# Kernel optimization log

Measured on AMD Instinct MI355X. Metric: run time of the kernel, lower is better.

The kernel has to match this reference:

```python
import jax, jax.numpy as jnp
import numpy as np

B, T, IN_CH, OUT_CH = 4, 512, 128, 128
NEG_INF = -1e22  # same large negative as the torch module


def setup_inputs() -> dict:
    key = jax.random.key(0)
    kx, ka, kq, kk, kp = jax.random.split(key, 5)
    x = jax.random.normal(kx, (B, T, IN_CH), dtype=jnp.float32)
    adj = jax.random.normal(ka, (B, T, T), dtype=jnp.float32)  # >0 -> edge
    # xavier-uniform-like scale for Linear weights (stored as (in, out) so y = x @ W)
    s_qk = float(np.sqrt(6.0 / (IN_CH + OUT_CH)))
    WQ = jax.random.uniform(kq, (IN_CH, OUT_CH), jnp.float32, -s_qk, s_qk)
    WK = jax.random.uniform(kk, (IN_CH, OUT_CH), jnp.float32, -s_qk, s_qk)
    s_p = float(np.sqrt(6.0 / (OUT_CH + 1)))
    p = jax.random.uniform(kp, (OUT_CH,), jnp.float32, -s_p, s_p)  # proj_att weight
    return {"x": x, "adj": adj, "WQ": WQ, "WK": WK, "p": p}


def reference(x, adj, WQ, WK, p):
    """Faithful LGCN forward (eval mode: dropout is identity).

    att[b,i,j] = p . relu(q[b,j] + k[b,i])   (note torch indexing:
    feat_q broadcast over dim 1, feat_k broadcast over dim 2)
    out[b,i]  = sum_j softmax_j(att + mask)[b,i,j] * x[b,j]
    """
    mask = jnp.where(adj > 0, jnp.float32(0.0), jnp.float32(NEG_INF))  # (B,T,T)
    q = x @ WQ  # (B,T,O)
    k = x @ WK  # (B,T,O)
    # (B, T_i, T_j, O): q indexed by j, k indexed by i
    h = jax.nn.relu(q[:, None, :, :] + k[:, :, None, :])
    score = jnp.einsum("bijd,d->bij", h, p)  # (B,T,T)
    att = jax.nn.softmax(score + mask, axis=-1)
    return jnp.matmul(att, x)  # (B,T,IN_CH)
```

## Files before the change

kernel.cpp:

```cpp
#include <hip/hip_runtime.h>

#define B_ 4
#define T_ 512
#define C_ 128
#define NEG_INF_ (-1e22f)
#define QSTRIDE 20

__global__ __launch_bounds__(256) void qk_gemm(const float* __restrict__ x,
                                               const float* __restrict__ WQ,
                                               const float* __restrict__ WK,
                                               float* __restrict__ q,
                                               float* __restrict__ k) {
    __shared__ float xs[C_][4];
    const int tid = threadIdx.x;
    const size_t rowbase = (size_t)blockIdx.x * 4 * C_;

    #pragma unroll
    for (int e = 0; e < 2; ++e) {
        int idx = e * 256 + tid;
        xs[idx & 127][idx >> 7] = x[rowbase + idx];
    }
    __syncthreads();

    const int m = tid >> 7;
    const int d = tid & 127;
    const float* __restrict__ W = m ? WK : WQ;
    float a0 = 0.f, a1 = 0.f, a2 = 0.f, a3 = 0.f;
    #pragma unroll 8
    for (int c = 0; c < C_; ++c) {
        float w = W[c * C_ + d];
        float4 xv = *(const float4*)&xs[c][0];
        a0 += xv.x * w; a1 += xv.y * w; a2 += xv.z * w; a3 += xv.w * w;
    }
    float* o = m ? k : q;
    o[rowbase + d]           = a0;
    o[rowbase + C_ + d]      = a1;
    o[rowbase + 2 * C_ + d]  = a2;
    o[rowbase + 3 * C_ + d]  = a3;
}

__global__ __launch_bounds__(256) void lgcn_att(const float* __restrict__ x,
                                                const float* __restrict__ adj,
                                                const float* __restrict__ q,
                                                const float* __restrict__ k,
                                                const float* __restrict__ p,
                                                float* __restrict__ out) {
    __shared__ float qs[512 * QSTRIDE];
    __shared__ float ks[4][C_];
    __shared__ float ps[C_];
    __shared__ float redm[4][4];
    __shared__ float reds[4][4];

    const int tid  = threadIdx.x;
    const int bid  = blockIdx.x;
    const int b    = bid >> 7;
    const int i0   = (bid & 127) << 2;
    const int wv   = tid >> 6;
    const int lane = tid & 63;
    const int jA   = tid;
    const int jB   = tid + 256;

    #pragma unroll
    for (int e = 0; e < 2; ++e) {
        int idx = e * 256 + tid;
        ks[idx >> 7][idx & 127] =
            k[((size_t)b * T_ + i0 + (idx >> 7)) * C_ + (idx & 127)];
    }
    if (tid < C_) ps[tid] = p[tid];

    float s4[4][2] = {{0.f, 0.f}, {0.f, 0.f}, {0.f, 0.f}, {0.f, 0.f}};
    const float* qb = q + (size_t)b * T_ * C_;

    for (int cd = 0; cd < 8; ++cd) {
        __syncthreads();
        #pragma unroll
        for (int it = 0; it < 8; ++it) {
            int idx = it * 256 + tid;
            int jj = idx >> 2, sl = idx & 3;
            float4 v = *(const float4*)&qb[(size_t)jj * C_ + cd * 16 + sl * 4];
            *(float4*)&qs[jj * QSTRIDE + sl * 4] = v;
        }
        __syncthreads();

        #pragma unroll
        for (int dl = 0; dl < 4; ++dl) {
            float4 qvA = *(const float4*)&qs[jA * QSTRIDE + dl * 4];
            float4 qvB = *(const float4*)&qs[jB * QSTRIDE + dl * 4];
            float4 pv  = *(const float4*)&ps[cd * 16 + dl * 4];
            #pragma unroll
            for (int r = 0; r < 4; ++r) {
                float4 kv = *(const float4*)&ks[r][cd * 16 + dl * 4];
                s4[r][0] += pv.x * fmaxf(qvA.x + kv.x, 0.f)
                          + pv.y * fmaxf(qvA.y + kv.y, 0.f)
                          + pv.z * fmaxf(qvA.z + kv.z, 0.f)
                          + pv.w * fmaxf(qvA.w + kv.w, 0.f);
                s4[r][1] += pv.x * fmaxf(qvB.x + kv.x, 0.f)
                          + pv.y * fmaxf(qvB.y + kv.y, 0.f)
                          + pv.z * fmaxf(qvB.z + kv.z, 0.f)
                          + pv.w * fmaxf(qvB.w + kv.w, 0.f);
            }
        }
    }

    const float* adjb = adj + ((size_t)b * T_ + i0) * T_;
    #pragma unroll
    for (int r = 0; r < 4; ++r) {
        float aA = adjb[(size_t)r * T_ + jA];
        float aB = adjb[(size_t)r * T_ + jB];
        s4[r][0] = (aA > 0.f) ? s4[r][0] : NEG_INF_;
        s4[r][1] = (aB > 0.f) ? s4[r][1] : NEG_INF_;
    }

    #pragma unroll
    for (int r = 0; r < 4; ++r) {
        float mv = fmaxf(s4[r][0], s4[r][1]);
        #pragma unroll
        for (int o = 32; o > 0; o >>= 1)
            mv = fmaxf(mv, __shfl_xor(mv, o, 64));
        if (lane == 0) redm[wv][r] = mv;
    }
    __syncthreads();
    float e4[4][2];
    #pragma unroll
    for (int r = 0; r < 4; ++r) {
        float rowmax = fmaxf(fmaxf(redm[0][r], redm[1][r]),
                             fmaxf(redm[2][r], redm[3][r]));
        e4[r][0] = __expf(s4[r][0] - rowmax);
        e4[r][1] = __expf(s4[r][1] - rowmax);
        float sm = e4[r][0] + e4[r][1];
        #pragma unroll
        for (int o = 32; o > 0; o >>= 1)
            sm += __shfl_xor(sm, o, 64);
        if (lane == 0) reds[wv][r] = sm;
    }

    float* outp = qs;
    const float2* xb2 = (const float2*)(x + (size_t)b * T_ * C_);
    float2 acc[4];
    #pragma unroll
    for (int r = 0; r < 4; ++r) acc[r] = make_float2(0.f, 0.f);
    const int jbase = wv * 64;
    #pragma unroll 2
    for (int l = 0; l < 64; ++l) {
        float2 xv0 = xb2[(size_t)(jbase + l) * 64 + lane];
        float2 xv1 = xb2[(size_t)(256 + jbase + l) * 64 + lane];
        #pragma unroll
        for (int r = 0; r < 4; ++r) {
            float a0 = __int_as_float(
                __builtin_amdgcn_readlane(__float_as_int(e4[r][0]), l));
            float a1 = __int_as_float(
                __builtin_amdgcn_readlane(__float_as_int(e4[r][1]), l));
            acc[r].x += a0 * xv0.x + a1 * xv1.x;
            acc[r].y += a0 * xv0.y + a1 * xv1.y;
        }
    }
    #pragma unroll
    for (int r = 0; r < 4; ++r)
        *(float2*)&outp[(wv * 4 + r) * C_ + lane * 2] = acc[r];
    __syncthreads();

    #pragma unroll
    for (int e = 0; e < 2; ++e) {
        const int row = (tid >> 7) + e * 2;
        const int d   = tid & 127;
        float v = outp[(0 * 4 + row) * C_ + d] + outp[(1 * 4 + row) * C_ + d]
                + outp[(2 * 4 + row) * C_ + d] + outp[(3 * 4 + row) * C_ + d];
        float denom = reds[0][row] + reds[1][row] + reds[2][row] + reds[3][row];
        out[((size_t)b * T_ + i0 + row) * C_ + d] = v / denom;
    }
}

extern "C" void kernel_launch(void* const* d_in, const int* in_sizes, int n_in,
                              void* d_out, int out_size, void* d_ws, size_t ws_size,
                              hipStream_t stream) {
    const float* x   = (const float*)d_in[0];
    const float* adj = (const float*)d_in[1];
    const float* WQ  = (const float*)d_in[2];
    const float* WK  = (const float*)d_in[3];
    const float* p   = (const float*)d_in[4];
    float* outp = (float*)d_out;

    float* q = (float*)d_ws;
    float* k = q + (size_t)B_ * T_ * C_;
    (void)ws_size; (void)in_sizes; (void)n_in;

    qk_gemm<<<512, 256, 0, stream>>>(x, WQ, WK, q, k);
    lgcn_att<<<512, 256, 0, stream>>>(x, adj, q, k, p, outp);
}
```

Measured before the change: 96.14 us.

## Load q rows directly into registers with prefetch instead of staging through LDS

Each thread now reads its two q rows straight from global memory into registers, prefetching the next 16-channel chunk while computing the current one. This removes the 40KB LDS staging buffer and the per-chunk barriers, which cuts LDS pressure and should raise occupancy. In exchange each thread issues strided row reads that are poorly coalesced across lanes and holds more registers.

```diff
diff --git a/kernel.cpp b/kernel.cpp
--- a/kernel.cpp
+++ b/kernel.cpp
@@ -4,7 +4,6 @@
 #define T_ 512
 #define C_ 128
 #define NEG_INF_ (-1e22f)
-#define QSTRIDE 20
 
 __global__ __launch_bounds__(256) void qk_gemm(const float* __restrict__ x,
                                                const float* __restrict__ WQ,
@@ -45,9 +44,9 @@
                                                 const float* __restrict__ k,
                                                 const float* __restrict__ p,
                                                 float* __restrict__ out) {
-    __shared__ float qs[512 * QSTRIDE];
     __shared__ float ks[4][C_];
     __shared__ float ps[C_];
+    __shared__ float outp[4][4][C_];
     __shared__ float redm[4][4];
     __shared__ float reds[4][4];
 
@@ -67,38 +66,50 @@
             k[((size_t)b * T_ + i0 + (idx >> 7)) * C_ + (idx & 127)];
     }
     if (tid < C_) ps[tid] = p[tid];
+    __syncthreads();
+
+    const float* qb    = q + (size_t)b * T_ * C_;
+    const float* qrowA = qb + (size_t)jA * C_;
+    const float* qrowB = qb + (size_t)jB * C_;
 
     float s4[4][2] = {{0.f, 0.f}, {0.f, 0.f}, {0.f, 0.f}, {0.f, 0.f}};
-    const float* qb = q + (size_t)b * T_ * C_;
 
+    float4 qa[4], qc[4];
+    #pragma unroll
+    for (int sl = 0; sl < 4; ++sl) {
+        qa[sl] = *(const float4*)&qrowA[sl * 4];
+        qc[sl] = *(const float4*)&qrowB[sl * 4];
+    }
+
+    #pragma unroll
     for (int cd = 0; cd < 8; ++cd) {
-        __syncthreads();
-        #pragma unroll
-        for (int it = 0; it < 8; ++it) {
-            int idx = it * 256 + tid;
-            int jj = idx >> 2, sl = idx & 3;
-            float4 v = *(const float4*)&qb[(size_t)jj * C_ + cd * 16 + sl * 4];
-            *(float4*)&qs[jj * QSTRIDE + sl * 4] = v;
+        float4 na[4], nc[4];
+        if (cd < 7) {
+            #pragma unroll
+            for (int sl = 0; sl < 4; ++sl) {
+                na[sl] = *(const float4*)&qrowA[(cd + 1) * 16 + sl * 4];
+                nc[sl] = *(const float4*)&qrowB[(cd + 1) * 16 + sl * 4];
+            }
         }
-        __syncthreads();
-
         #pragma unroll
         for (int dl = 0; dl < 4; ++dl) {
-            float4 qvA = *(const float4*)&qs[jA * QSTRIDE + dl * 4];
-            float4 qvB = *(const float4*)&qs[jB * QSTRIDE + dl * 4];
-            float4 pv  = *(const float4*)&ps[cd * 16 + dl * 4];
+            float4 pv = *(const float4*)&ps[cd * 16 + dl * 4];
             #pragma unroll
             for (int r = 0; r < 4; ++r) {
                 float4 kv = *(const float4*)&ks[r][cd * 16 + dl * 4];
-                s4[r][0] += pv.x * fmaxf(qvA.x + kv.x, 0.f)
-                          + pv.y * fmaxf(qvA.y + kv.y, 0.f)
-                          + pv.z * fmaxf(qvA.z + kv.z, 0.f)
-                          + pv.w * fmaxf(qvA.w + kv.w, 0.f);
-                s4[r][1] += pv.x * fmaxf(qvB.x + kv.x, 0.f)
-                          + pv.y * fmaxf(qvB.y + kv.y, 0.f)
-                          + pv.z * fmaxf(qvB.z + kv.z, 0.f)
-                          + pv.w * fmaxf(qvB.w + kv.w, 0.f);
+                s4[r][0] += pv.x * fmaxf(qa[dl].x + kv.x, 0.f)
+                          + pv.y * fmaxf(qa[dl].y + kv.y, 0.f)
+                          + pv.z * fmaxf(qa[dl].z + kv.z, 0.f)
+                          + pv.w * fmaxf(qa[dl].w + kv.w, 0.f);
+                s4[r][1] += pv.x * fmaxf(qc[dl].x + kv.x, 0.f)
+                          + pv.y * fmaxf(qc[dl].y + kv.y, 0.f)
+                          + pv.z * fmaxf(qc[dl].z + kv.z, 0.f)
+                          + pv.w * fmaxf(qc[dl].w + kv.w, 0.f);
             }
+        }
+        if (cd < 7) {
+            #pragma unroll
+            for (int sl = 0; sl < 4; ++sl) { qa[sl] = na[sl]; qc[sl] = nc[sl]; }
         }
     }
 
@@ -134,7 +145,6 @@
         if (lane == 0) reds[wv][r] = sm;
     }
 
-    float* outp = qs;
     const float2* xb2 = (const float2*)(x + (size_t)b * T_ * C_);
     float2 acc[4];
     #pragma unroll
@@ -156,15 +166,15 @@
     }
     #pragma unroll
     for (int r = 0; r < 4; ++r)
-        *(float2*)&outp[(wv * 4 + r) * C_ + lane * 2] = acc[r];
+        *(float2*)&outp[wv][r][lane * 2] = acc[r];
     __syncthreads();
 
     #pragma unroll
     for (int e = 0; e < 2; ++e) {
         const int row = (tid >> 7) + e * 2;
         const int d   = tid & 127;
-        float v = outp[(0 * 4 + row) * C_ + d] + outp[(1 * 4 + row) * C_ + d]
-                + outp[(2 * 4 + row) * C_ + d] + outp[(3 * 4 + row) * C_ + d];
+        float v = outp[0][row][d] + outp[1][row][d]
+                + outp[2][row][d] + outp[3][row][d];
         float denom = reds[0][row] + reds[1][row] + reds[2][row] + reds[3][row];
         out[((size_t)b * T_ + i0 + row) * C_ + d] = v / denom;
     }
```

Result: slower. 211.9 us (+120.4%).
